# Optimization experiments

Measured on AMD Instinct MI355X. Metric: run time of the kernel, lower is better.

Reference implementation:

```python
import jax, jax.numpy as jnp
import numpy as np

B, T, V, F = 64, 2, 512, 512  # V == F required by the original loop indexing

def setup_inputs() -> dict:
    key = jax.random.key(0)
    x = jax.random.normal(key, (B, T, V, F), dtype=jnp.float32)
    return {"x": x}

def reference(x):
    # split along time axis into two halves; only the first slice of the first half is used
    xh, _ = jnp.split(x, 2, axis=1)
    x0 = xh[:, 0]  # (B, V, F)
    # Faithful to tf.norm(x[:, 0, i, :], ord=2) with NO axis: Frobenius norm over
    # the whole (batch, feature) slice -> one scalar per vertex.
    n = jnp.sqrt(jnp.sum(x0 * x0, axis=(0, 2)))  # (V,)
    # S[b,i,j] = sum_f x0[b,i,f] * x0[b,j,f]  (inner loop over j covers all V since V==F)
    gram = jnp.einsum('bif,bjf->bij', x0, x0)  # (B, V, V)
    return gram / (n[:, None] * n[None, :])
```

## Files before the change

kernel.cpp:

```cpp
#include <hip/hip_runtime.h>
#include <hip/hip_bf16.h>
#include <math.h>


#define BATCH 64
#define VDIM 512
#define FDIM 512
#define XBS (2 * VDIM * FDIM)
#define OBS (VDIM * VDIM)

typedef __bf16 bf16x8 __attribute__((ext_vector_type(8)));
typedef __bf16 bf16x4 __attribute__((ext_vector_type(4)));
typedef float f32x4 __attribute__((ext_vector_type(4)));

#define BM 128
#define BK 64

#define INVN_OFF 33554432

#define GLL16(g, l)                                                          \
    __builtin_amdgcn_global_load_lds(                                        \
        (const __attribute__((address_space(1))) void*)(g),                  \
        (__attribute__((address_space(3))) void*)(l), 16, 0, 0)

__global__ __launch_bounds__(256) void cvt_norm_kernel(const float* __restrict__ x,
                                                       __bf16* __restrict__ xb,
                                                       float* __restrict__ inv_n) {
    const int v = blockIdx.x;
    const int tid = threadIdx.x;
    float s = 0.f;
    const float4* xf4 = (const float4*)x;
    for (int c = tid; c < 8192; c += 256) {
        int b = c >> 7;
        int f4 = c & 127;
        float4 d = xf4[(size_t)b * (XBS / 4) + (size_t)v * (FDIM / 4) + f4];
        s += d.x * d.x + d.y * d.y + d.z * d.z + d.w * d.w;
        bf16x4 p;
        p[0] = (__bf16)d.x; p[1] = (__bf16)d.y; p[2] = (__bf16)d.z; p[3] = (__bf16)d.w;
        *(bf16x4*)&xb[(size_t)b * (VDIM * FDIM) + (size_t)v * FDIM + f4 * 4] = p;
    }
    #pragma unroll
    for (int off = 32; off > 0; off >>= 1) s += __shfl_down(s, off, 64);
    __shared__ float partial[4];
    if ((tid & 63) == 0) partial[tid >> 6] = s;
    __syncthreads();
    if (tid == 0) {
        float t = partial[0] + partial[1] + partial[2] + partial[3];
        inv_n[v] = 1.0f / sqrtf(t);
    }
}

__global__ __launch_bounds__(256) void gram_kernel(const __bf16* __restrict__ xb,
                                                   const float* __restrict__ inv_n,
                                                   float* __restrict__ out) {
    __shared__ __bf16 As[BM * BK];
    __shared__ __bf16 Bs[BM * BK];

    const int bid = blockIdx.x;
    const int wg = (bid & 7) * 128 + (bid >> 3);
    const int batch = wg >> 4;
    const int tile = wg & 15;
    const int ti = tile >> 2;
    const int tj = tile & 3;

    const __bf16* xbb = xb + (size_t)batch * (VDIM * FDIM);
    const int tid = threadIdx.x;
    const int lane = tid & 63;
    const int wave = tid >> 6;
    const int wr = wave >> 1;
    const int wc = wave & 1;

    const __bf16* gA[4];
    const __bf16* gB[4];
    __bf16* la[4];
    __bf16* lb[4];
    #pragma unroll
    for (int it = 0; it < 4; ++it) {
        int c = it * 256 + tid;
        int row = c >> 3;
        int cs = (c & 7) ^ (row & 7);
        gA[it] = xbb + (size_t)(ti * BM + row) * FDIM + cs * 8;
        gB[it] = xbb + (size_t)(tj * BM + row) * FDIM + cs * 8;
        la[it] = &As[c * 8];
        lb[it] = &Bs[c * 8];
    }

    int offA[2][4], offB[2][4];
    #pragma unroll
    for (int ks = 0; ks < 2; ++ks) {
        #pragma unroll
        for (int m = 0; m < 4; ++m) {
            int rA = wr * 64 + m * 16 + (lane & 15);
            int rB = wc * 64 + m * 16 + (lane & 15);
            int gch = ks * 4 + (lane >> 4);
            offA[ks][m] = rA * (BK * 2) + ((gch ^ (rA & 7)) * 16);
            offB[ks][m] = rB * (BK * 2) + ((gch ^ (rB & 7)) * 16);
        }
    }

    f32x4 acc[4][4];
    #pragma unroll
    for (int m = 0; m < 4; ++m)
        #pragma unroll
        for (int n = 0; n < 4; ++n)
            acc[m][n] = (f32x4){0.f, 0.f, 0.f, 0.f};

    for (int kk = 0; kk < FDIM; kk += BK) {
        #pragma unroll
        for (int it = 0; it < 4; ++it) {
            GLL16(gA[it] + kk, la[it]);
            GLL16(gB[it] + kk, lb[it]);
        }
        __syncthreads();

        #pragma unroll
        for (int ks = 0; ks < 2; ++ks) {
            bf16x8 af[4], bfr[4];
            #pragma unroll
            for (int m = 0; m < 4; ++m) {
                af[m]  = *(const bf16x8*)((const char*)As + offA[ks][m]);
                bfr[m] = *(const bf16x8*)((const char*)Bs + offB[ks][m]);
            }
            #pragma unroll
            for (int m = 0; m < 4; ++m)
                #pragma unroll
                for (int n = 0; n < 4; ++n)
                    acc[m][n] = __builtin_amdgcn_mfma_f32_16x16x32_bf16(af[m], bfr[n], acc[m][n], 0, 0, 0);
        }
        __syncthreads();
    }

    const int rowbase = ti * BM + wr * 64;
    const int colbase = tj * BM + wc * 64;
    float* ob = out + (size_t)batch * OBS;

    float si[16];
    #pragma unroll
    for (int m = 0; m < 4; ++m)
        #pragma unroll
        for (int q = 0; q < 4; ++q)
            si[m * 4 + q] = inv_n[rowbase + m * 16 + (lane >> 4) * 4 + q];

    #pragma unroll
    for (int n = 0; n < 4; ++n) {
        int j = colbase + n * 16 + (lane & 15);
        float sj = inv_n[j];
        #pragma unroll
        for (int m = 0; m < 4; ++m) {
            #pragma unroll
            for (int q = 0; q < 4; ++q) {
                int i = rowbase + m * 16 + (lane >> 4) * 4 + q;
                ob[(size_t)i * VDIM + j] = acc[m][n][q] * si[m * 4 + q] * sj;
            }
        }
    }
}

extern "C" void kernel_launch(void* const* d_in, const int* in_sizes, int n_in,
                              void* d_out, int out_size, void* d_ws, size_t ws_size,
                              hipStream_t stream) {
    const float* x = (const float*)d_in[0];
    float* out = (float*)d_out;
    __bf16* xbf = (__bf16*)d_ws;
    float* inv_n = (float*)((char*)d_ws + INVN_OFF);

    cvt_norm_kernel<<<VDIM, 256, 0, stream>>>(x, xbf, inv_n);
    gram_kernel<<<BATCH * 16, 256, 0, stream>>>(xbf, inv_n, out);
}
```

Baseline: 50.06 us.

## Exploit Gram symmetry: compute upper-triangle tiles and mirror them via LDS transpose

The gram kernel now launches only the 10 upper-triangular 128x128 tiles per batch instead of all 16. For off-diagonal tiles it writes each result twice: once directly, and once transposed through a padded LDS buffer, reusing the A/B tile shared memory after the main loop. This cuts MFMA work and bf16 operand traffic by roughly a third, but the mirrored stores are only partly coalesced (64-byte row segments) and the grid is uneven across tile types. The normalisation is also folded into the accumulators once before the stores, and the convert/norm kernel now uses 512-thread blocks.

```diff
diff --git a/kernel.cpp b/kernel.cpp
--- a/kernel.cpp
+++ b/kernel.cpp
@@ -23,14 +23,14 @@
         (const __attribute__((address_space(1))) void*)(g),                  \
         (__attribute__((address_space(3))) void*)(l), 16, 0, 0)
 
-__global__ __launch_bounds__(256) void cvt_norm_kernel(const float* __restrict__ x,
+__global__ __launch_bounds__(512) void cvt_norm_kernel(const float* __restrict__ x,
                                                        __bf16* __restrict__ xb,
                                                        float* __restrict__ inv_n) {
     const int v = blockIdx.x;
     const int tid = threadIdx.x;
     float s = 0.f;
     const float4* xf4 = (const float4*)x;
-    for (int c = tid; c < 8192; c += 256) {
+    for (int c = tid; c < 8192; c += 512) {
         int b = c >> 7;
         int f4 = c & 127;
         float4 d = xf4[(size_t)b * (XBS / 4) + (size_t)v * (FDIM / 4) + f4];
@@ -41,11 +41,13 @@
     }
     #pragma unroll
     for (int off = 32; off > 0; off >>= 1) s += __shfl_down(s, off, 64);
-    __shared__ float partial[4];
+    __shared__ float partial[8];
     if ((tid & 63) == 0) partial[tid >> 6] = s;
     __syncthreads();
     if (tid == 0) {
-        float t = partial[0] + partial[1] + partial[2] + partial[3];
+        float t = 0.f;
+        #pragma unroll
+        for (int w = 0; w < 8; ++w) t += partial[w];
         inv_n[v] = 1.0f / sqrtf(t);
     }
 }
@@ -57,11 +59,13 @@
     __shared__ __bf16 Bs[BM * BK];
 
     const int bid = blockIdx.x;
-    const int wg = (bid & 7) * 128 + (bid >> 3);
-    const int batch = wg >> 4;
-    const int tile = wg & 15;
-    const int ti = tile >> 2;
-    const int tj = tile & 3;
+    const int wg = (bid & 7) * 80 + (bid >> 3);
+    const int batch = wg / 10;
+    const int t = wg - batch * 10;
+    const int TI[10] = {0, 0, 0, 0, 1, 1, 1, 2, 2, 3};
+    const int TJ[10] = {0, 1, 2, 3, 1, 2, 3, 2, 3, 3};
+    const int ti = TI[t];
+    const int tj = TJ[t];
 
     const __bf16* xbb = xb + (size_t)batch * (VDIM * FDIM);
     const int tid = threadIdx.x;
@@ -134,23 +138,56 @@
     const int colbase = tj * BM + wc * 64;
     float* ob = out + (size_t)batch * OBS;
 
-    float si[16];
+    float si[16], sj[4];
     #pragma unroll
     for (int m = 0; m < 4; ++m)
         #pragma unroll
         for (int q = 0; q < 4; ++q)
             si[m * 4 + q] = inv_n[rowbase + m * 16 + (lane >> 4) * 4 + q];
+    #pragma unroll
+    for (int n = 0; n < 4; ++n)
+        sj[n] = inv_n[colbase + n * 16 + (lane & 15)];
+    #pragma unroll
+    for (int m = 0; m < 4; ++m)
+        #pragma unroll
+        for (int n = 0; n < 4; ++n)
+            #pragma unroll
+            for (int q = 0; q < 4; ++q)
+                acc[m][n][q] *= si[m * 4 + q] * sj[n];
 
     #pragma unroll
     for (int n = 0; n < 4; ++n) {
         int j = colbase + n * 16 + (lane & 15);
-        float sj = inv_n[j];
-        #pragma unroll
-        for (int m = 0; m < 4; ++m) {
+        #pragma unroll
+        for (int m = 0; m < 4; ++m)
             #pragma unroll
             for (int q = 0; q < 4; ++q) {
                 int i = rowbase + m * 16 + (lane >> 4) * 4 + q;
-                ob[(size_t)i * VDIM + j] = acc[m][n][q] * si[m * 4 + q] * sj;
+                ob[(size_t)i * VDIM + j] = acc[m][n][q];
+            }
+    }
+
+    if (ti != tj) {
+        float* tbase = (wave < 2) ? (float*)As : (float*)Bs;
+        float* tb = tbase + (wave & 1) * 1088;
+        const int j16 = lane >> 2;
+        const int ic = lane & 3;
+        #pragma unroll
+        for (int n = 0; n < 4; ++n) {
+            #pragma unroll
+            for (int m = 0; m < 4; ++m)
+                #pragma unroll
+                for (int q = 0; q < 4; ++q)
+                    tb[(m * 16 + (lane >> 4) * 4 + q) * 17 + (lane & 15)] = acc[m][n][q];
+            #pragma unroll
+            for (int c = 0; c < 4; ++c) {
+                f32x4 v4;
+                #pragma unroll
+                for (int e = 0; e < 4; ++e)
+                    v4[e] = tb[(ic * 16 + c * 4 + e) * 17 + j16];
+                int J = colbase + n * 16 + j16;
+                int I = rowbase + ic * 16 + c * 4;
+                *(f32x4*)&ob[(size_t)J * VDIM + I] = v4;
             }
         }
     }
@@ -164,6 +201,6 @@
     __bf16* xbf = (__bf16*)d_ws;
     float* inv_n = (float*)((char*)d_ws + INVN_OFF);
 
-    cvt_norm_kernel<<<VDIM, 256, 0, stream>>>(x, xbf, inv_n);
-    gram_kernel<<<BATCH * 16, 256, 0, stream>>>(xbf, inv_n, out);
+    cvt_norm_kernel<<<VDIM, 512, 0, stream>>>(x, xbf, inv_n);
+    gram_kernel<<<BATCH * 10, 256, 0, stream>>>(xbf, inv_n, out);
 }
```

New measurement: 52.06 us. +4.0%, slower.

## Double-buffer LDS tiles in gram kernel and widen cvt_norm blocks

Applied to the files above, without the earlier changes.

The gram kernel now keeps two LDS buffers for A and B tiles and issues the global-to-LDS loads for the next K tile before computing on the current one. It uses explicit vmcnt waits and raw barriers so the copy overlaps the MFMA work, and fully unrolls the K loop. LDS use doubles to 64KB per block, which may lower occupancy. Separately, the conversion/norm kernel runs with 512 threads per block instead of 256.

```diff
diff --git a/kernel.cpp b/kernel.cpp
--- a/kernel.cpp
+++ b/kernel.cpp
@@ -15,6 +15,7 @@
 
 #define BM 128
 #define BK 64
+#define NKT (FDIM / BK)
 
 #define INVN_OFF 33554432
 
@@ -23,14 +24,14 @@
         (const __attribute__((address_space(1))) void*)(g),                  \
         (__attribute__((address_space(3))) void*)(l), 16, 0, 0)
 
-__global__ __launch_bounds__(256) void cvt_norm_kernel(const float* __restrict__ x,
+__global__ __launch_bounds__(512) void cvt_norm_kernel(const float* __restrict__ x,
                                                        __bf16* __restrict__ xb,
                                                        float* __restrict__ inv_n) {
     const int v = blockIdx.x;
     const int tid = threadIdx.x;
     float s = 0.f;
     const float4* xf4 = (const float4*)x;
-    for (int c = tid; c < 8192; c += 256) {
+    for (int c = tid; c < 8192; c += 512) {
         int b = c >> 7;
         int f4 = c & 127;
         float4 d = xf4[(size_t)b * (XBS / 4) + (size_t)v * (FDIM / 4) + f4];
@@ -41,11 +42,13 @@
     }
     #pragma unroll
     for (int off = 32; off > 0; off >>= 1) s += __shfl_down(s, off, 64);
-    __shared__ float partial[4];
+    __shared__ float partial[8];
     if ((tid & 63) == 0) partial[tid >> 6] = s;
     __syncthreads();
     if (tid == 0) {
-        float t = partial[0] + partial[1] + partial[2] + partial[3];
+        float t = 0.f;
+        #pragma unroll
+        for (int w = 0; w < 8; ++w) t += partial[w];
         inv_n[v] = 1.0f / sqrtf(t);
     }
 }
@@ -53,8 +56,8 @@
 __global__ __launch_bounds__(256) void gram_kernel(const __bf16* __restrict__ xb,
                                                    const float* __restrict__ inv_n,
                                                    float* __restrict__ out) {
-    __shared__ __bf16 As[BM * BK];
-    __shared__ __bf16 Bs[BM * BK];
+    __shared__ __bf16 As[2][BM * BK];
+    __shared__ __bf16 Bs[2][BM * BK];
 
     const int bid = blockIdx.x;
     const int wg = (bid & 7) * 128 + (bid >> 3);
@@ -72,8 +75,7 @@
 
     const __bf16* gA[4];
     const __bf16* gB[4];
-    __bf16* la[4];
-    __bf16* lb[4];
+    int ldsoff[4];
     #pragma unroll
     for (int it = 0; it < 4; ++it) {
         int c = it * 256 + tid;
@@ -81,8 +83,7 @@
         int cs = (c & 7) ^ (row & 7);
         gA[it] = xbb + (size_t)(ti * BM + row) * FDIM + cs * 8;
         gB[it] = xbb + (size_t)(tj * BM + row) * FDIM + cs * 8;
-        la[it] = &As[c * 8];
-        lb[it] = &Bs[c * 8];
+        ldsoff[it] = c * 8;
     }
 
     int offA[2][4], offB[2][4];
@@ -105,21 +106,36 @@
         for (int n = 0; n < 4; ++n)
             acc[m][n] = (f32x4){0.f, 0.f, 0.f, 0.f};
 
-    for (int kk = 0; kk < FDIM; kk += BK) {
-        #pragma unroll
-        for (int it = 0; it < 4; ++it) {
-            GLL16(gA[it] + kk, la[it]);
-            GLL16(gB[it] + kk, lb[it]);
+    #pragma unroll
+    for (int it = 0; it < 4; ++it) {
+        GLL16(gA[it], &As[0][ldsoff[it]]);
+        GLL16(gB[it], &Bs[0][ldsoff[it]]);
+    }
+
+    #pragma unroll
+    for (int t = 0; t < NKT; ++t) {
+        if (t < NKT - 1) {
+            const int nb = (t + 1) & 1;
+            #pragma unroll
+            for (int it = 0; it < 4; ++it) {
+                GLL16(gA[it] + (t + 1) * BK, &As[nb][ldsoff[it]]);
+                GLL16(gB[it] + (t + 1) * BK, &Bs[nb][ldsoff[it]]);
+            }
+            asm volatile("s_waitcnt vmcnt(8)" ::: "memory");
+        } else {
+            asm volatile("s_waitcnt vmcnt(0)" ::: "memory");
         }
-        __syncthreads();
+        __builtin_amdgcn_s_barrier();
 
+        const char* Ab = (const char*)&As[t & 1][0];
+        const char* Bb = (const char*)&Bs[t & 1][0];
         #pragma unroll
         for (int ks = 0; ks < 2; ++ks) {
             bf16x8 af[4], bfr[4];
             #pragma unroll
             for (int m = 0; m < 4; ++m) {
-                af[m]  = *(const bf16x8*)((const char*)As + offA[ks][m]);
-                bfr[m] = *(const bf16x8*)((const char*)Bs + offB[ks][m]);
+                af[m]  = *(const bf16x8*)(Ab + offA[ks][m]);
+                bfr[m] = *(const bf16x8*)(Bb + offB[ks][m]);
             }
             #pragma unroll
             for (int m = 0; m < 4; ++m)
@@ -127,7 +143,8 @@
                 for (int n = 0; n < 4; ++n)
                     acc[m][n] = __builtin_amdgcn_mfma_f32_16x16x32_bf16(af[m], bfr[n], acc[m][n], 0, 0, 0);
         }
-        __syncthreads();
+        asm volatile("s_waitcnt lgkmcnt(0)" ::: "memory");
+        __builtin_amdgcn_s_barrier();
     }
 
     const int rowbase = ti * BM + wr * 64;
@@ -164,6 +181,6 @@
     __bf16* xbf = (__bf16*)d_ws;
     float* inv_n = (float*)((char*)d_ws + INVN_OFF);
 
-    cvt_norm_kernel<<<VDIM, 256, 0, stream>>>(x, xbf, inv_n);
+    cvt_norm_kernel<<<VDIM, 512, 0, stream>>>(x, xbf, inv_n);
     gram_kernel<<<BATCH * 16, 256, 0, stream>>>(xbf, inv_n, out);
 }
```

Measured after the change: 55.27 us. 10.4% more time.

## Fuse convert/norm and gram into one cooperative kernel with double-buffered 256x256 tiles

Applied to the files above, without the earlier changes.

Replaces the two-kernel pipeline with a single cooperative kernel of 256 blocks. Each block first converts its slice of x to bf16 and accumulates squared norms through LDS and global atomics, then the whole grid syncs before the GEMM. The GEMM phase moves to 256x256 tiles with 512 threads and double-buffered global-to-LDS loads, waiting on vmcnt so the next stage's loads overlap the current MFMAs. It adds a memset launch, atomics and a grid-wide barrier, and the larger tiles leave only 256 blocks to fill the machine.

```diff
diff --git a/kernel.cpp b/kernel.cpp
--- a/kernel.cpp
+++ b/kernel.cpp
@@ -1,6 +1,9 @@
 #include <hip/hip_runtime.h>
 #include <hip/hip_bf16.h>
+#include <hip/hip_cooperative_groups.h>
 #include <math.h>
+
+namespace cg = cooperative_groups;
 
 
 #define BATCH 64
@@ -13,140 +16,143 @@
 typedef __bf16 bf16x4 __attribute__((ext_vector_type(4)));
 typedef float f32x4 __attribute__((ext_vector_type(4)));
 
-#define BM 128
-#define BK 64
-
-#define INVN_OFF 33554432
+#define NSQ_OFF 33554432
 
 #define GLL16(g, l)                                                          \
     __builtin_amdgcn_global_load_lds(                                        \
         (const __attribute__((address_space(1))) void*)(g),                  \
         (__attribute__((address_space(3))) void*)(l), 16, 0, 0)
 
-__global__ __launch_bounds__(256) void cvt_norm_kernel(const float* __restrict__ x,
-                                                       __bf16* __restrict__ xb,
-                                                       float* __restrict__ inv_n) {
-    const int v = blockIdx.x;
-    const int tid = threadIdx.x;
-    float s = 0.f;
-    const float4* xf4 = (const float4*)x;
-    for (int c = tid; c < 8192; c += 256) {
-        int b = c >> 7;
-        int f4 = c & 127;
-        float4 d = xf4[(size_t)b * (XBS / 4) + (size_t)v * (FDIM / 4) + f4];
-        s += d.x * d.x + d.y * d.y + d.z * d.z + d.w * d.w;
-        bf16x4 p;
-        p[0] = (__bf16)d.x; p[1] = (__bf16)d.y; p[2] = (__bf16)d.z; p[3] = (__bf16)d.w;
-        *(bf16x4*)&xb[(size_t)b * (VDIM * FDIM) + (size_t)v * FDIM + f4 * 4] = p;
-    }
-    #pragma unroll
-    for (int off = 32; off > 0; off >>= 1) s += __shfl_down(s, off, 64);
-    __shared__ float partial[4];
-    if ((tid & 63) == 0) partial[tid >> 6] = s;
-    __syncthreads();
-    if (tid == 0) {
-        float t = partial[0] + partial[1] + partial[2] + partial[3];
-        inv_n[v] = 1.0f / sqrtf(t);
-    }
-}
-
-__global__ __launch_bounds__(256) void gram_kernel(const __bf16* __restrict__ xb,
-                                                   const float* __restrict__ inv_n,
-                                                   float* __restrict__ out) {
-    __shared__ __bf16 As[BM * BK];
-    __shared__ __bf16 Bs[BM * BK];
+__global__ __launch_bounds__(512, 2) void fused_kernel(const float* __restrict__ x,
+                                                       __bf16* __restrict__ ws,
+                                                       float* __restrict__ nsq,
+                                                       float* __restrict__ out) {
+    __shared__ __bf16 As[2][16384];
+    __shared__ __bf16 Bs[2][16384];
+    __shared__ float nsq_l[128];
 
     const int bid = blockIdx.x;
-    const int wg = (bid & 7) * 128 + (bid >> 3);
-    const int batch = wg >> 4;
-    const int tile = wg & 15;
-    const int ti = tile >> 2;
-    const int tj = tile & 3;
-
-    const __bf16* xbb = xb + (size_t)batch * (VDIM * FDIM);
+    const int L = (bid & 7) * 32 + (bid >> 3);
     const int tid = threadIdx.x;
     const int lane = tid & 63;
     const int wave = tid >> 6;
-    const int wr = wave >> 1;
-    const int wc = wave & 1;
 
+    {
+        const int b = L >> 2;
+        const int q = L & 3;
+        if (tid < 128) nsq_l[tid] = 0.f;
+        __syncthreads();
+        const float4* src = (const float4*)(x + (size_t)b * XBS + (size_t)q * 128 * FDIM);
+        bf16x4* dst = (bf16x4*)(ws + (size_t)b * (VDIM * FDIM) + (size_t)q * 128 * FDIM);
+        const int row_w = wave >> 1;
+        #pragma unroll 4
+        for (int i = 0; i < 32; ++i) {
+            int c = i * 512 + tid;
+            float4 d = src[c];
+            bf16x4 p;
+            p[0] = (__bf16)d.x; p[1] = (__bf16)d.y; p[2] = (__bf16)d.z; p[3] = (__bf16)d.w;
+            dst[c] = p;
+            float s = d.x * d.x + d.y * d.y + d.z * d.z + d.w * d.w;
+            #pragma unroll
+            for (int off = 32; off > 0; off >>= 1) s += __shfl_down(s, off, 64);
+            if (lane == 0) atomicAdd(&nsq_l[i * 4 + row_w], s);
+        }
+        __syncthreads();
+        if (tid < 128) atomicAdd(&nsq[q * 128 + tid], nsq_l[tid]);
+    }
+
+    cg::this_grid().sync();
+
+    const int batch = L >> 2;
+    const int tile = L & 3;
+    const int tr = tile >> 1;
+    const int tc = tile & 1;
+    const __bf16* wsb = ws + (size_t)batch * (VDIM * FDIM);
+    const int wr = wave >> 2;
+    const int wc = wave & 3;
+
+    const int r0 = tid >> 3;
+    const int cc = tid & 7;
     const __bf16* gA[4];
     const __bf16* gB[4];
-    __bf16* la[4];
-    __bf16* lb[4];
+    int lo[4];
     #pragma unroll
-    for (int it = 0; it < 4; ++it) {
-        int c = it * 256 + tid;
-        int row = c >> 3;
-        int cs = (c & 7) ^ (row & 7);
-        gA[it] = xbb + (size_t)(ti * BM + row) * FDIM + cs * 8;
-        gB[it] = xbb + (size_t)(tj * BM + row) * FDIM + cs * 8;
-        la[it] = &As[c * 8];
-        lb[it] = &Bs[c * 8];
+    for (int j = 0; j < 4; ++j) {
+        int row = j * 64 + r0;
+        int cs = cc ^ (row & 7);
+        gA[j] = wsb + (size_t)(tr * 256 + row) * FDIM + cs * 8;
+        gB[j] = wsb + (size_t)(tc * 256 + row) * FDIM + cs * 8;
+        lo[j] = (j * 512 + tid) * 8;
     }
 
-    int offA[2][4], offB[2][4];
+    auto stage = [&](int kt) {
+        const int nb = kt & 1;
+        #pragma unroll
+        for (int j = 0; j < 4; ++j) GLL16(gA[j] + kt * 64, &As[nb][lo[j]]);
+        #pragma unroll
+        for (int j = 0; j < 4; ++j) GLL16(gB[j] + kt * 64, &Bs[nb][lo[j]]);
+    };
+
+    const int gs0 = (lane >> 4) ^ (lane & 7);
+    const int abase = (wr * 128 + (lane & 15)) * 128 + gs0 * 16;
+    const int bbase = (wc * 64 + (lane & 15)) * 128 + gs0 * 16;
+
+    f32x4 acc[8][4];
     #pragma unroll
-    for (int ks = 0; ks < 2; ++ks) {
-        #pragma unroll
-        for (int m = 0; m < 4; ++m) {
-            int rA = wr * 64 + m * 16 + (lane & 15);
-            int rB = wc * 64 + m * 16 + (lane & 15);
-            int gch = ks * 4 + (lane >> 4);
-            offA[ks][m] = rA * (BK * 2) + ((gch ^ (rA & 7)) * 16);
-            offB[ks][m] = rB * (BK * 2) + ((gch ^ (rB & 7)) * 16);
-        }
-    }
-
-    f32x4 acc[4][4];
-    #pragma unroll
-    for (int m = 0; m < 4; ++m)
+    for (int m = 0; m < 8; ++m)
         #pragma unroll
         for (int n = 0; n < 4; ++n)
             acc[m][n] = (f32x4){0.f, 0.f, 0.f, 0.f};
 
-    for (int kk = 0; kk < FDIM; kk += BK) {
-        #pragma unroll
-        for (int it = 0; it < 4; ++it) {
-            GLL16(gA[it] + kk, la[it]);
-            GLL16(gB[it] + kk, lb[it]);
+    stage(0);
+    #pragma unroll
+    for (int kt = 0; kt < 8; ++kt) {
+        if (kt < 7) {
+            stage(kt + 1);
+            asm volatile("s_waitcnt vmcnt(8)" ::: "memory");
+        } else {
+            asm volatile("s_waitcnt vmcnt(0)" ::: "memory");
         }
-        __syncthreads();
+        __builtin_amdgcn_s_barrier();
 
+        const char* Ab = (const char*)&As[kt & 1][0];
+        const char* Bb = (const char*)&Bs[kt & 1][0];
         #pragma unroll
         for (int ks = 0; ks < 2; ++ks) {
-            bf16x8 af[4], bfr[4];
+            bf16x8 af[8], bfr[4];
             #pragma unroll
-            for (int m = 0; m < 4; ++m) {
-                af[m]  = *(const bf16x8*)((const char*)As + offA[ks][m]);
-                bfr[m] = *(const bf16x8*)((const char*)Bs + offB[ks][m]);
-            }
+            for (int m = 0; m < 8; ++m)
+                af[m] = *(const bf16x8*)(Ab + ((abase + m * 2048) ^ (ks * 64)));
             #pragma unroll
-            for (int m = 0; m < 4; ++m)
+            for (int n = 0; n < 4; ++n)
+                bfr[n] = *(const bf16x8*)(Bb + ((bbase + n * 2048) ^ (ks * 64)));
+            #pragma unroll
+            for (int m = 0; m < 8; ++m)
                 #pragma unroll
                 for (int n = 0; n < 4; ++n)
                     acc[m][n] = __builtin_amdgcn_mfma_f32_16x16x32_bf16(af[m], bfr[n], acc[m][n], 0, 0, 0);
         }
-        __syncthreads();
+        asm volatile("s_waitcnt lgkmcnt(0)" ::: "memory");
+        __builtin_amdgcn_s_barrier();
     }
 
-    const int rowbase = ti * BM + wr * 64;
-    const int colbase = tj * BM + wc * 64;
+    const int rowbase = tr * 256 + wr * 128;
+    const int colbase = tc * 256 + wc * 64;
     float* ob = out + (size_t)batch * OBS;
 
-    float si[16];
+    float si[32];
     #pragma unroll
-    for (int m = 0; m < 4; ++m)
+    for (int m = 0; m < 8; ++m)
         #pragma unroll
         for (int q = 0; q < 4; ++q)
-            si[m * 4 + q] = inv_n[rowbase + m * 16 + (lane >> 4) * 4 + q];
+            si[m * 4 + q] = rsqrtf(nsq[rowbase + m * 16 + (lane >> 4) * 4 + q]);
 
     #pragma unroll
     for (int n = 0; n < 4; ++n) {
         int j = colbase + n * 16 + (lane & 15);
-        float sj = inv_n[j];
+        float sj = rsqrtf(nsq[j]);
         #pragma unroll
-        for (int m = 0; m < 4; ++m) {
+        for (int m = 0; m < 8; ++m) {
             #pragma unroll
             for (int q = 0; q < 4; ++q) {
                 int i = rowbase + m * 16 + (lane >> 4) * 4 + q;
@@ -161,9 +167,12 @@
                               hipStream_t stream) {
     const float* x = (const float*)d_in[0];
     float* out = (float*)d_out;
-    __bf16* xbf = (__bf16*)d_ws;
-    float* inv_n = (float*)((char*)d_ws + INVN_OFF);
+    __bf16* ws = (__bf16*)d_ws;
+    float* nsq = (float*)((char*)d_ws + NSQ_OFF);
 
-    cvt_norm_kernel<<<VDIM, 256, 0, stream>>>(x, xbf, inv_n);
-    gram_kernel<<<BATCH * 16, 256, 0, stream>>>(xbf, inv_n, out);
+    hipMemsetAsync(nsq, 0, VDIM * sizeof(float), stream);
+
+    void* args[] = {(void*)&x, (void*)&ws, (void*)&nsq, (void*)&out};
+    hipLaunchCooperativeKernel((const void*)fused_kernel, dim3(256), dim3(512),
+                               args, 0, stream);
 }
```

New measurement: 94.85 us. 89.5% more time.
